# Kernel tuning notes

Measured on AMD Instinct MI355X. Metric: run time of the kernel, lower is better.

Reference implementation:

```python
import jax, jax.numpy as jnp
import numpy as np

N_HEADS = 16
DIMS = 1024
HEAD_SIZE = DIMS // N_HEADS


def setup_inputs() -> dict:
    key = jax.random.key(0)
    k1, k2, k3, k4, k5 = jax.random.split(key, 5)
    x = jax.random.normal(k1, (1, 4096, DIMS), dtype=jnp.float32)
    s = 1.0 / np.sqrt(DIMS)
    w_qkv = jax.random.uniform(k2, (3 * DIMS, DIMS), jnp.float32, -s, s)
    b_qkv = jax.random.uniform(k3, (3 * DIMS,), jnp.float32, -s, s)
    w_o = jax.random.uniform(k4, (DIMS, DIMS), jnp.float32, -s, s)
    b_o = jax.random.uniform(k5, (DIMS,), jnp.float32, -s, s)
    return {"x": x, "w_qkv": w_qkv, "b_qkv": b_qkv, "w_o": w_o, "b_o": b_o,
            "causal_mask": 1}


def reference(x, w_qkv, b_qkv, w_o, b_o, causal_mask):
    B, S, D = x.shape
    qkv = x @ w_qkv.T + b_qkv                      # [B,S,3D]
    q, k, v = jnp.split(qkv, 3, axis=-1)
    def heads(t):
        return t.reshape(B, S, N_HEADS, HEAD_SIZE).transpose(0, 2, 1, 3)  # [B,H,S,hd]
    q, k, v = heads(q), heads(k), heads(v)
    scores = jnp.einsum("bhsd,bhtd->bhst", q, k)   # [B,H,S,S]
    if causal_mask:
        tri = jnp.triu(jnp.ones((S, S), dtype=bool), k=1)
        scores = jnp.where(tri, -jnp.inf, scores)  # mask BEFORE scale, as in torch code
    scores = scores / np.sqrt(HEAD_SIZE)
    weights = jax.nn.softmax(scores, axis=-1)
    out = jnp.einsum("bhst,bhtd->bhsd", weights, v)  # [B,H,S,hd]
    out = out.transpose(0, 2, 1, 3).reshape(B, S, D)
    return out @ w_o.T + b_o
```

## Files before the change

### kernel.cpp

```cpp
#include <hip/hip_runtime.h>
#include <hip/hip_bf16.h>
#include <stdint.h>

typedef __attribute__((ext_vector_type(8))) short short8;
typedef __attribute__((ext_vector_type(4))) float f32x4;
typedef __hip_bfloat16 bf16;

#define S_LEN 4096
#define DMODEL 1024
#define NH 16
#define HD 64
#define QSCALE 0.1803368801111f

static __device__ inline uint2 pack4(float4 v) {
  union { uint2 u; bf16 h[4]; } p;
  p.h[0] = (bf16)v.x; p.h[1] = (bf16)v.y; p.h[2] = (bf16)v.z; p.h[3] = (bf16)v.w;
  return p.u;
}

static __device__ inline void gload_lds16(const bf16* g, bf16* l) {
  __builtin_amdgcn_global_load_lds(
      (const __attribute__((address_space(1))) unsigned int*)g,
      (__attribute__((address_space(3))) unsigned int*)l, 16, 0, 0);
}

template <int CTRL>
static __device__ inline float dpp_rorf(float x) {
  int r = __builtin_amdgcn_update_dpp(0, __builtin_bit_cast(int, x),
                                      CTRL, 0xf, 0xf, true);
  return __builtin_bit_cast(float, r);
}
static __device__ inline float row16_sum(float x) {
  x += dpp_rorf<0x121>(x);
  x += dpp_rorf<0x122>(x);
  x += dpp_rorf<0x124>(x);
  x += dpp_rorf<0x128>(x);
  return x;
}

static __device__ inline int rot_idx(int r, int c) {
  return r * 64 + ((c + ((r & 7) << 3)) & 63);
}

__global__ __launch_bounds__(256)
void cvt_all(const float* __restrict__ x, const float* __restrict__ wq,
             const float* __restrict__ wo, bf16* __restrict__ xb,
             bf16* __restrict__ wqb, bf16* __restrict__ wob) {
  const int nx = S_LEN * DMODEL;
  const int nq = 3 * DMODEL * DMODEL;
  const int no = DMODEL * DMODEL;
  int i = (blockIdx.x * 256 + threadIdx.x) * 4;
  if (i < nx) {
    *(uint2*)(xb + i) = pack4(*(const float4*)(x + i));
  } else if (i < nx + nq) {
    int j = i - nx;
    *(uint2*)(wqb + j) = pack4(*(const float4*)(wq + j));
  } else if (i < nx + nq + no) {
    int j = i - nx - nq;
    *(uint2*)(wob + j) = pack4(*(const float4*)(wo + j));
  }
}

__global__ __launch_bounds__(256)
void gemm_qkv(const bf16* __restrict__ A, const bf16* __restrict__ B,
              const float* __restrict__ bias, bf16* __restrict__ qkv2,
              bf16* __restrict__ vt) {
  const int K = DMODEL;
  __shared__ bf16 sA[128 * 64];
  __shared__ bf16 sB[128 * 64];
  const int tid  = threadIdx.x;
  const int lane = tid & 63;
  const int wave = tid >> 6;
  const int wm = wave >> 1, wn = wave & 1;
  const int tileM = blockIdx.y * 128;
  const int tileN = blockIdx.x * 128;

  const int lrow = lane & 15;
  const int quad = lane >> 4;
  const int kq   = quad * 8;

  f32x4 acc[4][4];
#pragma unroll
  for (int i = 0; i < 4; i++)
#pragma unroll
    for (int j = 0; j < 4; j++) acc[i][j] = (f32x4){0.f, 0.f, 0.f, 0.f};

  const int trl = lane >> 3;
  const int cgl = (((lane & 7) - trl) & 7) << 3;
  const bf16* aP[4];
  const bf16* bP[4];
#pragma unroll
  for (int c = 0; c < 4; c++) {
    int ch = wave * 4 + c;
    aP[c] = A + (size_t)(tileM + ch * 8 + trl) * K + cgl;
    bP[c] = B + (size_t)(tileN + ch * 8 + trl) * K + cgl;
  }

  for (int k0 = 0; k0 < K; k0 += 64) {
    __syncthreads();
#pragma unroll
    for (int c = 0; c < 4; c++) {
      int ch = wave * 4 + c;
      gload_lds16(aP[c] + k0, sA + ch * 512);
      gload_lds16(bP[c] + k0, sB + ch * 512);
    }
    __syncthreads();
#pragma unroll
    for (int ks = 0; ks < 2; ks++) {
      short8 afrag[4], bfrag[4];
#pragma unroll
      for (int mi = 0; mi < 4; mi++)
        afrag[mi] = *(const short8*)(sA + rot_idx(wm * 64 + mi * 16 + lrow, ks * 32 + kq));
#pragma unroll
      for (int ni = 0; ni < 4; ni++)
        bfrag[ni] = *(const short8*)(sB + rot_idx(wn * 64 + ni * 16 + lrow, ks * 32 + kq));
#pragma unroll
      for (int mi = 0; mi < 4; mi++)
#pragma unroll
        for (int ni = 0; ni < 4; ni++)
          acc[mi][ni] = __builtin_amdgcn_mfma_f32_16x16x32_bf16(afrag[mi], bfrag[ni], acc[mi][ni], 0, 0, 0);
    }
  }

#pragma unroll
  for (int ni = 0; ni < 4; ni++) {
    int col = tileN + wn * 64 + ni * 16 + lrow;
    float bv = bias[col];
    if (col < 2 * DMODEL) {
      float sc = (col < DMODEL) ? QSCALE : 1.0f;
#pragma unroll
      for (int mi = 0; mi < 4; mi++) {
        int row0 = tileM + wm * 64 + mi * 16 + quad * 4;
#pragma unroll
        for (int r = 0; r < 4; r++)
          qkv2[(size_t)(row0 + r) * 2048 + col] = (bf16)((acc[mi][ni][r] + bv) * sc);
      }
    } else {
      int cc = col - 2 * DMODEL;
      int hh = cc >> 6, dd = cc & 63;
      bf16* vrow = vt + ((size_t)(hh * 64 + dd)) * S_LEN;
#pragma unroll
      for (int mi = 0; mi < 4; mi++) {
        int row0 = tileM + wm * 64 + mi * 16 + quad * 4;
        float4 v = {acc[mi][ni][0] + bv, acc[mi][ni][1] + bv,
                    acc[mi][ni][2] + bv, acc[mi][ni][3] + bv};
        *(uint2*)(vrow + row0) = pack4(v);
      }
    }
  }
}

__global__ __launch_bounds__(256)
void gemm_oproj(const bf16* __restrict__ A, const bf16* __restrict__ B,
                const float* __restrict__ bias, float* __restrict__ C) {
  const int K = DMODEL, N = DMODEL;
  __shared__ bf16 sA[128 * 64];
  __shared__ bf16 sB[64 * 64];
  const int tid  = threadIdx.x;
  const int lane = tid & 63;
  const int wave = tid >> 6;
  const int wm = wave >> 1, wn = wave & 1;
  const int tileM = blockIdx.y * 128;
  const int tileN = blockIdx.x * 64;

  const int lrow = lane & 15;
  const int quad = lane >> 4;
  const int kq   = quad * 8;

  f32x4 acc[4][2];
#pragma unroll
  for (int i = 0; i < 4; i++)
#pragma unroll
    for (int j = 0; j < 2; j++) acc[i][j] = (f32x4){0.f, 0.f, 0.f, 0.f};

  const int trl = lane >> 3;
  const int cgl = (((lane & 7) - trl) & 7) << 3;
  const bf16* aP[4];
  const bf16* bP[2];
#pragma unroll
  for (int c = 0; c < 4; c++) {
    int ch = wave * 4 + c;
    aP[c] = A + (size_t)(tileM + ch * 8 + trl) * K + cgl;
  }
#pragma unroll
  for (int c = 0; c < 2; c++) {
    int ch = wave * 2 + c;
    bP[c] = B + (size_t)(tileN + ch * 8 + trl) * K + cgl;
  }

  for (int k0 = 0; k0 < K; k0 += 64) {
    __syncthreads();
#pragma unroll
    for (int c = 0; c < 4; c++)
      gload_lds16(aP[c] + k0, sA + (wave * 4 + c) * 512);
#pragma unroll
    for (int c = 0; c < 2; c++)
      gload_lds16(bP[c] + k0, sB + (wave * 2 + c) * 512);
    __syncthreads();
#pragma unroll
    for (int ks = 0; ks < 2; ks++) {
      short8 afrag[4], bfrag[2];
#pragma unroll
      for (int mi = 0; mi < 4; mi++)
        afrag[mi] = *(const short8*)(sA + rot_idx(wm * 64 + mi * 16 + lrow, ks * 32 + kq));
#pragma unroll
      for (int ni = 0; ni < 2; ni++)
        bfrag[ni] = *(const short8*)(sB + rot_idx(wn * 32 + ni * 16 + lrow, ks * 32 + kq));
#pragma unroll
      for (int mi = 0; mi < 4; mi++)
#pragma unroll
        for (int ni = 0; ni < 2; ni++)
          acc[mi][ni] = __builtin_amdgcn_mfma_f32_16x16x32_bf16(afrag[mi], bfrag[ni], acc[mi][ni], 0, 0, 0);
    }
  }

#pragma unroll
  for (int ni = 0; ni < 2; ni++) {
    int col = tileN + wn * 32 + ni * 16 + lrow;
    float bv = bias[col];
#pragma unroll
    for (int mi = 0; mi < 4; mi++) {
      int row0 = tileM + wm * 64 + mi * 16 + quad * 4;
#pragma unroll
      for (int r = 0; r < 4; r++)
        C[(size_t)(row0 + r) * N + col] = acc[mi][ni][r] + bv;
    }
  }
}

__global__ __launch_bounds__(256)
void gemm_qkv_f32(const float* __restrict__ A, const float* __restrict__ B,
                  const float* __restrict__ bias, bf16* __restrict__ qkv2,
                  bf16* __restrict__ vt) {
  const int K = DMODEL;
  __shared__ bf16 sA[128 * 64];
  __shared__ bf16 sB[128 * 64];
  const int tid  = threadIdx.x;
  const int lane = tid & 63;
  const int wave = tid >> 6;
  const int wm = wave >> 1, wn = wave & 1;
  const int tileM = blockIdx.y * 128;
  const int tileN = blockIdx.x * 128;
  const int lrow = lane & 15;
  const int quad = lane >> 4;
  const int kq   = quad * 8;

  f32x4 acc[4][4];
#pragma unroll
  for (int i = 0; i < 4; i++)
#pragma unroll
    for (int j = 0; j < 4; j++) acc[i][j] = (f32x4){0.f, 0.f, 0.f, 0.f};

  const int r0 = tid >> 4;
  const int cc = (tid & 15) * 4;

  for (int k0 = 0; k0 < K; k0 += 64) {
    uint2 ra[8], rb[8];
#pragma unroll
    for (int i = 0; i < 8; i++) {
      int row = r0 + i * 16;
      ra[i] = pack4(*(const float4*)(A + (size_t)(tileM + row) * K + k0 + cc));
      rb[i] = pack4(*(const float4*)(B + (size_t)(tileN + row) * K + k0 + cc));
    }
    __syncthreads();
#pragma unroll
    for (int i = 0; i < 8; i++) {
      int row = r0 + i * 16;
      *(uint2*)(sA + row * 64 + cc) = ra[i];
      *(uint2*)(sB + row * 64 + cc) = rb[i];
    }
    __syncthreads();
#pragma unroll
    for (int ks = 0; ks < 2; ks++) {
      short8 afrag[4], bfrag[4];
#pragma unroll
      for (int mi = 0; mi < 4; mi++)
        afrag[mi] = *(const short8*)(sA + (wm * 64 + mi * 16 + lrow) * 64 + ks * 32 + kq);
#pragma unroll
      for (int ni = 0; ni < 4; ni++)
        bfrag[ni] = *(const short8*)(sB + (wn * 64 + ni * 16 + lrow) * 64 + ks * 32 + kq);
#pragma unroll
      for (int mi = 0; mi < 4; mi++)
#pragma unroll
        for (int ni = 0; ni < 4; ni++)
          acc[mi][ni] = __builtin_amdgcn_mfma_f32_16x16x32_bf16(afrag[mi], bfrag[ni], acc[mi][ni], 0, 0, 0);
    }
  }
#pragma unroll
  for (int ni = 0; ni < 4; ni++) {
    int col = tileN + wn * 64 + ni * 16 + lrow;
    float bv = bias[col];
    if (col < 2 * DMODEL) {
      float sc = (col < DMODEL) ? QSCALE : 1.0f;
#pragma unroll
      for (int mi = 0; mi < 4; mi++) {
        int row0 = tileM + wm * 64 + mi * 16 + quad * 4;
#pragma unroll
        for (int r = 0; r < 4; r++)
          qkv2[(size_t)(row0 + r) * 2048 + col] = (bf16)((acc[mi][ni][r] + bv) * sc);
      }
    } else {
      int c2 = col - 2 * DMODEL;
      int hh = c2 >> 6, dd = c2 & 63;
      bf16* vrow = vt + ((size_t)(hh * 64 + dd)) * S_LEN;
#pragma unroll
      for (int mi = 0; mi < 4; mi++) {
        int row0 = tileM + wm * 64 + mi * 16 + quad * 4;
        float4 v = {acc[mi][ni][0] + bv, acc[mi][ni][1] + bv,
                    acc[mi][ni][2] + bv, acc[mi][ni][3] + bv};
        *(uint2*)(vrow + row0) = pack4(v);
      }
    }
  }
}

__global__ __launch_bounds__(256)
void gemm_oproj_f32w(const bf16* __restrict__ A, const float* __restrict__ B,
                     const float* __restrict__ bias, float* __restrict__ C) {
  const int K = DMODEL, N = DMODEL;
  __shared__ bf16 sA[128 * 64];
  __shared__ bf16 sB[128 * 64];
  const int tid  = threadIdx.x;
  const int lane = tid & 63;
  const int wave = tid >> 6;
  const int wm = wave >> 1, wn = wave & 1;
  const int tileM = blockIdx.y * 128;
  const int tileN = blockIdx.x * 128;
  const int lrow = lane & 15;
  const int quad = lane >> 4;
  const int kq   = quad * 8;

  f32x4 acc[4][4];
#pragma unroll
  for (int i = 0; i < 4; i++)
#pragma unroll
    for (int j = 0; j < 4; j++) acc[i][j] = (f32x4){0.f, 0.f, 0.f, 0.f};

  const int a_r0 = tid >> 3;
  const int a_cc = (tid & 7) * 8;
  const int b_r0 = tid >> 4;
  const int b_cc = (tid & 15) * 4;

  for (int k0 = 0; k0 < K; k0 += 64) {
    uint4 ra[4];
    uint2 rb[8];
#pragma unroll
    for (int i = 0; i < 4; i++)
      ra[i] = *(const uint4*)(A + (size_t)(tileM + a_r0 + i * 32) * K + k0 + a_cc);
#pragma unroll
    for (int i = 0; i < 8; i++)
      rb[i] = pack4(*(const float4*)(B + (size_t)(tileN + b_r0 + i * 16) * K + k0 + b_cc));
    __syncthreads();
#pragma unroll
    for (int i = 0; i < 4; i++)
      *(uint4*)(sA + (a_r0 + i * 32) * 64 + a_cc) = ra[i];
#pragma unroll
    for (int i = 0; i < 8; i++)
      *(uint2*)(sB + (b_r0 + i * 16) * 64 + b_cc) = rb[i];
    __syncthreads();
#pragma unroll
    for (int ks = 0; ks < 2; ks++) {
      short8 afrag[4], bfrag[4];
#pragma unroll
      for (int mi = 0; mi < 4; mi++)
        afrag[mi] = *(const short8*)(sA + (wm * 64 + mi * 16 + lrow) * 64 + ks * 32 + kq);
#pragma unroll
      for (int ni = 0; ni < 4; ni++)
        bfrag[ni] = *(const short8*)(sB + (wn * 64 + ni * 16 + lrow) * 64 + ks * 32 + kq);
#pragma unroll
      for (int mi = 0; mi < 4; mi++)
#pragma unroll
        for (int ni = 0; ni < 4; ni++)
          acc[mi][ni] = __builtin_amdgcn_mfma_f32_16x16x32_bf16(afrag[mi], bfrag[ni], acc[mi][ni], 0, 0, 0);
    }
  }
#pragma unroll
  for (int ni = 0; ni < 4; ni++) {
    int col = tileN + wn * 64 + ni * 16 + lrow;
    float bv = bias[col];
#pragma unroll
    for (int mi = 0; mi < 4; mi++) {
      int row0 = tileM + wm * 64 + mi * 16 + quad * 4;
#pragma unroll
      for (int r = 0; r < 4; r++)
        C[(size_t)(row0 + r) * N + col] = acc[mi][ni][r] + bv;
    }
  }
}

__global__ __launch_bounds__(256, 4)
void attn_kernel(const bf16* __restrict__ qkv2, const bf16* __restrict__ vt,
                 bf16* __restrict__ attn_out, const int* __restrict__ causal_ptr) {
  __shared__ bf16 sQP[64 * 64];
  __shared__ bf16 sK[2][64 * 64];
  __shared__ bf16 sV[2][64 * 64];

  const int tid  = threadIdx.x;
  const int lane = tid & 63;
  const int wave = tid >> 6;
  const int h  = blockIdx.y;
  const int qi = (h < 8) ? (int)blockIdx.x : (63 - (int)blockIdx.x);
  const int qbase = qi * 64;
  const bool causal = (*causal_ptr) != 0;

  const int lrow = lane & 15;
  const int quad = lane >> 4;
  const int kq   = quad * 8;

  const int trl = lane >> 3;
  const int cgl = (((lane & 7) - trl) & 7) << 3;

  const bf16* Qb = qkv2 + h * HD;
  const bf16* Kb = qkv2 + DMODEL + h * HD;
  const bf16* Vb = vt + (size_t)(h * HD) * S_LEN;

#pragma unroll
  for (int i = 0; i < 2; i++) {
    int ch = wave * 2 + i;
    int row = ch * 8 + trl;
    gload_lds16(Qb + (size_t)(qbase + row) * 2048 + cgl, sQP + ch * 512);
  }
#pragma unroll
  for (int i = 0; i < 2; i++) {
    int ch = wave * 2 + i;
    int trow = ch * 8 + trl;
    gload_lds16(Kb + (size_t)trow * 2048 + cgl, sK[0] + ch * 512);
    gload_lds16(Vb + (size_t)trow * S_LEN + cgl, sV[0] + ch * 512);
  }

  f32x4 oacc[4];
#pragma unroll
  for (int ni = 0; ni < 4; ni++) oacc[ni] = (f32x4){0.f, 0.f, 0.f, 0.f};
  float l_st[4] = {0.f, 0.f, 0.f, 0.f};

  const int nkt = causal ? (qi + 1) : (S_LEN / 64);
  const int wave_row_min = qbase + wave * 16;
  bf16* sPw = sQP + wave * (16 * 64);

  __syncthreads();
  short8 qf[2];
#pragma unroll
  for (int ks = 0; ks < 2; ks++)
    qf[ks] = *(const short8*)(sQP + rot_idx(wave * 16 + lrow, ks * 32 + kq));

  for (int jt = 0; jt < nkt; jt++) {
    const int cur = jt & 1;
    const int kbase = jt * 64;
    __syncthreads();

    if (jt + 1 < nkt) {
      const int kb2 = kbase + 64;
#pragma unroll
      for (int i = 0; i < 2; i++) {
        int ch = wave * 2 + i;
        int trow = ch * 8 + trl;
        gload_lds16(Kb + (size_t)(kb2 + trow) * 2048 + cgl, sK[cur ^ 1] + ch * 512);
        gload_lds16(Vb + (size_t)trow * S_LEN + kb2 + cgl, sV[cur ^ 1] + ch * 512);
      }
    }

    f32x4 sacc[4];
#pragma unroll
    for (int ni = 0; ni < 4; ni++) sacc[ni] = (f32x4){0.f, 0.f, 0.f, 0.f};
#pragma unroll
    for (int ks = 0; ks < 2; ks++) {
      short8 kf[4];
#pragma unroll
      for (int ni = 0; ni < 4; ni++)
        kf[ni] = *(const short8*)(sK[cur] + rot_idx(ni * 16 + lrow, ks * 32 + kq));
#pragma unroll
      for (int ni = 0; ni < 4; ni++)
        sacc[ni] = __builtin_amdgcn_mfma_f32_16x16x32_bf16(qf[ks], kf[ni], sacc[ni], 0, 0, 0);
    }

    const bool need_mask = causal && (kbase + 63 > wave_row_min);
#pragma unroll
    for (int r = 0; r < 4; r++) {
      const int row_l = quad * 4 + r;
      const int row_g = qbase + wave * 16 + row_l;
      float psum = 0.f;
#pragma unroll
      for (int ni = 0; ni < 4; ni++) {
        float p = __builtin_amdgcn_exp2f(sacc[ni][r]);
        if (need_mask && (kbase + ni * 16 + lrow > row_g)) p = 0.f;
        sPw[rot_idx(row_l, ni * 16 + lrow)] = (bf16)p;
        psum += p;
      }
      l_st[r] += psum;
    }

#pragma unroll
    for (int ks = 0; ks < 2; ks++) {
      short8 pf, vf[4];
      pf = *(const short8*)(sPw + rot_idx(lrow, ks * 32 + kq));
#pragma unroll
      for (int ni = 0; ni < 4; ni++)
        vf[ni] = *(const short8*)(sV[cur] + rot_idx(ni * 16 + lrow, ks * 32 + kq));
#pragma unroll
      for (int ni = 0; ni < 4; ni++)
        oacc[ni] = __builtin_amdgcn_mfma_f32_16x16x32_bf16(pf, vf[ni], oacc[ni], 0, 0, 0);
    }
  }

#pragma unroll
  for (int r = 0; r < 4; r++) {
    float l = row16_sum(l_st[r]);
    float inv = 1.0f / fmaxf(l, 1e-30f);
    int row_g = qbase + wave * 16 + quad * 4 + r;
#pragma unroll
    for (int ni = 0; ni < 4; ni++) {
      int col = h * HD + ni * 16 + lrow;
      attn_out[(size_t)row_g * DMODEL + col] = (bf16)(oacc[ni][r] * inv);
    }
  }
}

extern "C" void kernel_launch(void* const* d_in, const int* in_sizes, int n_in,
                              void* d_out, int out_size, void* d_ws, size_t ws_size,
                              hipStream_t stream) {
  const float* x     = (const float*)d_in[0];
  const float* w_qkv = (const float*)d_in[1];
  const float* b_qkv = (const float*)d_in[2];
  const float* w_o   = (const float*)d_in[3];
  const float* b_o   = (const float*)d_in[4];
  const int*   cm    = (const int*)d_in[5];

  char* ws = (char*)d_ws;
  bf16* qkv2 = (bf16*)ws;
  bf16* vt   = (bf16*)(ws + 16777216);
  bf16* attn = (bf16*)(ws + 25165824);
  bf16* xb   = (bf16*)(ws + 33554432);
  bf16* wqb  = (bf16*)(ws + 41943040);
  bf16* wob  = (bf16*)(ws + 48234496);

  dim3 blk(256);
  const bool fast = (ws_size >= (size_t)50331648);

  if (fast) {
    const int ntot = S_LEN * DMODEL + 3 * DMODEL * DMODEL + DMODEL * DMODEL;
    cvt_all<<<dim3((ntot / 4 + 255) / 256), blk, 0, stream>>>(
        x, w_qkv, w_o, xb, wqb, wob);
    gemm_qkv<<<dim3(3 * DMODEL / 128, S_LEN / 128), blk, 0, stream>>>(
        xb, wqb, b_qkv, qkv2, vt);
    attn_kernel<<<dim3(S_LEN / 64, NH), blk, 0, stream>>>(qkv2, vt, attn, cm);
    gemm_oproj<<<dim3(DMODEL / 64, S_LEN / 128), blk, 0, stream>>>(
        attn, wob, b_o, (float*)d_out);
  } else {
    gemm_qkv_f32<<<dim3(3 * DMODEL / 128, S_LEN / 128), blk, 0, stream>>>(
        x, w_qkv, b_qkv, qkv2, vt);
    attn_kernel<<<dim3(S_LEN / 64, NH), blk, 0, stream>>>(qkv2, vt, attn, cm);
    gemm_oproj_f32w<<<dim3(DMODEL / 128, S_LEN / 128), blk, 0, stream>>>(
        attn, w_o, b_o, (float*)d_out);
  }
}
```

Before: 224.8 us.

## Restructure attention to 128-row Q tiles with 32x32 MFMA and register-resident P

The attention kernel now processes 128 query rows per block, with 32 rows per wave, using 32x32x16 bf16 MFMAs and computing S^T so the probabilities can be repacked in registers via cross-half shuffles. This removes the round trip of P through LDS. Each K/V tile loaded into LDS is reused by twice as many query rows, and fully masked 32- or 16-column chunks are skipped. The row-sum reduction now goes through LDS, and launch bounds drop to 2 blocks per SIMD to allow more registers, which halves the grid and may reduce occupancy and load balance.

```diff
diff --git a/kernel.cpp b/kernel.cpp
--- a/kernel.cpp
+++ b/kernel.cpp
@@ -4,6 +4,7 @@
 
 typedef __attribute__((ext_vector_type(8))) short short8;
 typedef __attribute__((ext_vector_type(4))) float f32x4;
+typedef __attribute__((ext_vector_type(16))) float f32x16;
 typedef __hip_bfloat16 bf16;
 
 #define S_LEN 4096
@@ -18,24 +19,16 @@
   return p.u;
 }
 
+static __device__ inline uint32_t pack2(float a, float b) {
+  union { uint32_t u; bf16 h[2]; } p;
+  p.h[0] = (bf16)a; p.h[1] = (bf16)b;
+  return p.u;
+}
+
 static __device__ inline void gload_lds16(const bf16* g, bf16* l) {
   __builtin_amdgcn_global_load_lds(
       (const __attribute__((address_space(1))) unsigned int*)g,
       (__attribute__((address_space(3))) unsigned int*)l, 16, 0, 0);
-}
-
-template <int CTRL>
-static __device__ inline float dpp_rorf(float x) {
-  int r = __builtin_amdgcn_update_dpp(0, __builtin_bit_cast(int, x),
-                                      CTRL, 0xf, 0xf, true);
-  return __builtin_bit_cast(float, r);
-}
-static __device__ inline float row16_sum(float x) {
-  x += dpp_rorf<0x121>(x);
-  x += dpp_rorf<0x122>(x);
-  x += dpp_rorf<0x124>(x);
-  x += dpp_rorf<0x128>(x);
-  return x;
 }
 
 static __device__ inline int rot_idx(int r, int c) {
@@ -388,10 +381,10 @@
   }
 }
 
-__global__ __launch_bounds__(256, 4)
+__global__ __launch_bounds__(256, 2)
 void attn_kernel(const bf16* __restrict__ qkv2, const bf16* __restrict__ vt,
                  bf16* __restrict__ attn_out, const int* __restrict__ causal_ptr) {
-  __shared__ bf16 sQP[64 * 64];
+  __shared__ bf16 sQ[128 * 64];
   __shared__ bf16 sK[2][64 * 64];
   __shared__ bf16 sV[2][64 * 64];
 
@@ -399,13 +392,12 @@
   const int lane = tid & 63;
   const int wave = tid >> 6;
   const int h  = blockIdx.y;
-  const int qi = (h < 8) ? (int)blockIdx.x : (63 - (int)blockIdx.x);
-  const int qbase = qi * 64;
+  const int qi = (h < 8) ? (int)blockIdx.x : (31 - (int)blockIdx.x);
+  const int qbase = qi * 128;
   const bool causal = (*causal_ptr) != 0;
 
-  const int lrow = lane & 15;
-  const int quad = lane >> 4;
-  const int kq   = quad * 8;
+  const int l31 = lane & 31;
+  const int hi  = lane >> 5;
 
   const int trl = lane >> 3;
   const int cgl = (((lane & 7) - trl) & 7) << 3;
@@ -415,10 +407,9 @@
   const bf16* Vb = vt + (size_t)(h * HD) * S_LEN;
 
 #pragma unroll
-  for (int i = 0; i < 2; i++) {
-    int ch = wave * 2 + i;
-    int row = ch * 8 + trl;
-    gload_lds16(Qb + (size_t)(qbase + row) * 2048 + cgl, sQP + ch * 512);
+  for (int i = 0; i < 4; i++) {
+    int ch = wave * 4 + i;
+    gload_lds16(Qb + (size_t)(qbase + ch * 8 + trl) * 2048 + cgl, sQ + ch * 512);
   }
 #pragma unroll
   for (int i = 0; i < 2; i++) {
@@ -428,20 +419,23 @@
     gload_lds16(Vb + (size_t)trow * S_LEN + cgl, sV[0] + ch * 512);
   }
 
-  f32x4 oacc[4];
-#pragma unroll
-  for (int ni = 0; ni < 4; ni++) oacc[ni] = (f32x4){0.f, 0.f, 0.f, 0.f};
-  float l_st[4] = {0.f, 0.f, 0.f, 0.f};
-
-  const int nkt = causal ? (qi + 1) : (S_LEN / 64);
-  const int wave_row_min = qbase + wave * 16;
-  bf16* sPw = sQP + wave * (16 * 64);
+  f32x16 oacc[2];
+#pragma unroll
+  for (int nc = 0; nc < 2; nc++)
+#pragma unroll
+    for (int e = 0; e < 16; e++) oacc[nc][e] = 0.f;
+  float l_st = 0.f;
+
+  const int nkt = causal ? (2 * qi + 2) : (S_LEN / 64);
+  const int wrmin = qbase + wave * 32;
+  const int wrmax = wrmin + 31;
+  const int q_g   = wrmin + l31;
 
   __syncthreads();
-  short8 qf[2];
-#pragma unroll
-  for (int ks = 0; ks < 2; ks++)
-    qf[ks] = *(const short8*)(sQP + rot_idx(wave * 16 + lrow, ks * 32 + kq));
+  short8 qf[4];
+#pragma unroll
+  for (int kd = 0; kd < 4; kd++)
+    qf[kd] = *(const short8*)(sQ + rot_idx(wave * 32 + l31, kd * 16 + hi * 8));
 
   for (int jt = 0; jt < nkt; jt++) {
     const int cur = jt & 1;
@@ -458,59 +452,95 @@
         gload_lds16(Vb + (size_t)trow * S_LEN + kb2 + cgl, sV[cur ^ 1] + ch * 512);
       }
     }
-
-    f32x4 sacc[4];
-#pragma unroll
-    for (int ni = 0; ni < 4; ni++) sacc[ni] = (f32x4){0.f, 0.f, 0.f, 0.f};
-#pragma unroll
-    for (int ks = 0; ks < 2; ks++) {
-      short8 kf[4];
-#pragma unroll
-      for (int ni = 0; ni < 4; ni++)
-        kf[ni] = *(const short8*)(sK[cur] + rot_idx(ni * 16 + lrow, ks * 32 + kq));
-#pragma unroll
-      for (int ni = 0; ni < 4; ni++)
-        sacc[ni] = __builtin_amdgcn_mfma_f32_16x16x32_bf16(qf[ks], kf[ni], sacc[ni], 0, 0, 0);
-    }
-
-    const bool need_mask = causal && (kbase + 63 > wave_row_min);
-#pragma unroll
-    for (int r = 0; r < 4; r++) {
-      const int row_l = quad * 4 + r;
-      const int row_g = qbase + wave * 16 + row_l;
-      float psum = 0.f;
-#pragma unroll
-      for (int ni = 0; ni < 4; ni++) {
-        float p = __builtin_amdgcn_exp2f(sacc[ni][r]);
-        if (need_mask && (kbase + ni * 16 + lrow > row_g)) p = 0.f;
-        sPw[rot_idx(row_l, ni * 16 + lrow)] = (bf16)p;
-        psum += p;
-      }
-      l_st[r] += psum;
-    }
-
-#pragma unroll
-    for (int ks = 0; ks < 2; ks++) {
-      short8 pf, vf[4];
-      pf = *(const short8*)(sPw + rot_idx(lrow, ks * 32 + kq));
-#pragma unroll
-      for (int ni = 0; ni < 4; ni++)
-        vf[ni] = *(const short8*)(sV[cur] + rot_idx(ni * 16 + lrow, ks * 32 + kq));
-#pragma unroll
-      for (int ni = 0; ni < 4; ni++)
-        oacc[ni] = __builtin_amdgcn_mfma_f32_16x16x32_bf16(pf, vf[ni], oacc[ni], 0, 0, 0);
-    }
-  }
-
-#pragma unroll
-  for (int r = 0; r < 4; r++) {
-    float l = row16_sum(l_st[r]);
-    float inv = 1.0f / fmaxf(l, 1e-30f);
-    int row_g = qbase + wave * 16 + quad * 4 + r;
-#pragma unroll
-    for (int ni = 0; ni < 4; ni++) {
-      int col = h * HD + ni * 16 + lrow;
-      attn_out[(size_t)row_g * DMODEL + col] = (bf16)(oacc[ni][r] * inv);
+    if (causal && kbase > wrmax) continue;
+
+    uint32_t pw[4][4];
+#pragma unroll
+    for (int kc = 0; kc < 2; kc++) {
+      if (causal && (kbase + kc * 32 > wrmax)) {
+#pragma unroll
+        for (int w = 0; w < 4; w++) { pw[kc * 2][w] = 0u; pw[kc * 2 + 1][w] = 0u; }
+      } else {
+        f32x16 sacc;
+#pragma unroll
+        for (int e = 0; e < 16; e++) sacc[e] = 0.f;
+#pragma unroll
+        for (int kd = 0; kd < 4; kd++) {
+          short8 kf = *(const short8*)(sK[cur] + rot_idx(kc * 32 + l31, kd * 16 + hi * 8));
+          sacc = __builtin_amdgcn_mfma_f32_32x32x16_bf16(kf, qf[kd], sacc, 0, 0, 0);
+        }
+        const bool nm = causal && (kbase + kc * 32 + 31 > wrmin);
+        float p[16];
+        float psum = 0.f;
+#pragma unroll
+        for (int g = 0; g < 4; g++) {
+#pragma unroll
+          for (int r = 0; r < 4; r++) {
+            float v = __builtin_amdgcn_exp2f(sacc[g * 4 + r]);
+            if (nm) {
+              int kg = kbase + kc * 32 + g * 8 + hi * 4 + r;
+              if (kg > q_g) v = 0.f;
+            }
+            p[g * 4 + r] = v;
+            psum += v;
+          }
+        }
+        l_st += psum;
+        uint32_t pku[4][2];
+#pragma unroll
+        for (int g = 0; g < 4; g++) {
+#pragma unroll
+          for (int h2 = 0; h2 < 2; h2++)
+            pku[g][h2] = pack2(p[g * 4 + h2 * 2], p[g * 4 + h2 * 2 + 1]);
+        }
+#pragma unroll
+        for (int c2 = 0; c2 < 2; c2++) {
+#pragma unroll
+          for (int h2 = 0; h2 < 2; h2++) {
+            uint32_t a = pku[2 * c2][h2], b = pku[2 * c2 + 1][h2];
+            uint32_t sa = (uint32_t)__shfl_xor((int)a, 32);
+            uint32_t sb = (uint32_t)__shfl_xor((int)b, 32);
+            pw[kc * 2 + c2][h2]     = hi ? sb : a;
+            pw[kc * 2 + c2][2 + h2] = hi ? b  : sa;
+          }
+        }
+      }
+    }
+
+#pragma unroll
+    for (int kk = 0; kk < 4; kk++) {
+      if (causal && (kbase + kk * 16 > wrmax)) continue;
+      union { short8 s; uint32_t u[4]; } pf;
+#pragma unroll
+      for (int w = 0; w < 4; w++) pf.u[w] = pw[kk][w];
+#pragma unroll
+      for (int nc = 0; nc < 2; nc++) {
+        short8 vf = *(const short8*)(sV[cur] + rot_idx(nc * 32 + l31, kk * 16 + hi * 8));
+        oacc[nc] = __builtin_amdgcn_mfma_f32_32x32x16_bf16(pf.s, vf, oacc[nc], 0, 0, 0);
+      }
+    }
+  }
+
+  float ltot = l_st + __shfl_xor(l_st, 32);
+  float* l_lds = (float*)sQ;
+  if (hi == 0) l_lds[wave * 32 + l31] = ltot;
+  float invl[4][4];
+#pragma unroll
+  for (int g = 0; g < 4; g++) {
+    f32x4 lv = *(const f32x4*)(l_lds + wave * 32 + g * 8 + hi * 4);
+#pragma unroll
+    for (int r = 0; r < 4; r++) invl[g][r] = 1.0f / fmaxf(lv[r], 1e-30f);
+  }
+#pragma unroll
+  for (int nc = 0; nc < 2; nc++) {
+#pragma unroll
+    for (int g = 0; g < 4; g++) {
+#pragma unroll
+      for (int r = 0; r < 4; r++) {
+        int qg = qbase + wave * 32 + g * 8 + hi * 4 + r;
+        int col = h * HD + nc * 32 + l31;
+        attn_out[(size_t)qg * DMODEL + col] = (bf16)(oacc[nc][g * 4 + r] * invl[g][r]);
+      }
     }
   }
 }
@@ -542,13 +572,13 @@
         x, w_qkv, w_o, xb, wqb, wob);
     gemm_qkv<<<dim3(3 * DMODEL / 128, S_LEN / 128), blk, 0, stream>>>(
         xb, wqb, b_qkv, qkv2, vt);
-    attn_kernel<<<dim3(S_LEN / 64, NH), blk, 0, stream>>>(qkv2, vt, attn, cm);
+    attn_kernel<<<dim3(S_LEN / 128, NH), blk, 0, stream>>>(qkv2, vt, attn, cm);
     gemm_oproj<<<dim3(DMODEL / 64, S_LEN / 128), blk, 0, stream>>>(
         attn, wob, b_o, (float*)d_out);
   } else {
     gemm_qkv_f32<<<dim3(3 * DMODEL / 128, S_LEN / 128), blk, 0, stream>>>(
         x, w_qkv, b_qkv, qkv2, vt);
-    attn_kernel<<<dim3(S_LEN / 64, NH), blk, 0, stream>>>(qkv2, vt, attn, cm);
+    attn_kernel<<<dim3(S_LEN / 128, NH), blk, 0, stream>>>(qkv2, vt, attn, cm);
     gemm_oproj_f32w<<<dim3(DMODEL / 128, S_LEN / 128), blk, 0, stream>>>(
         attn, w_o, b_o, (float*)d_out);
   }
```

After: 256.1 us. 1.14x slower.
